# Kernel tuning notes

Measured on AMD Instinct MI355X. Metric: run time of the kernel, lower is better.

## Reference

```python
import jax, jax.numpy as jnp
import numpy as np

HEADS = 4
DIM_HEAD = 32
SCALE = 10.0  # scale=10 init arg
HIDDEN = HEADS * DIM_HEAD


def _l2norm(t, eps=1e-12):
    # matches torch F.normalize(t, dim=-1): normalize over last axis (flattened spatial)
    n = jnp.sqrt(jnp.sum(t * t, axis=-1, keepdims=True))
    return t / jnp.maximum(n, eps)


def setup_inputs() -> dict:
    key = jax.random.key(0)
    k1, k2, k3, k4, k5 = jax.random.split(key, 5)
    b, dim, H, W = 2, 128, 64, 64
    x = jax.random.normal(k1, (b, dim, H, W), jnp.float32)
    y = jax.random.normal(k2, (b, dim, H, W), jnp.float32)
    # to_qkv: Conv2d(dim, 3*hidden, 1, bias=False) -> weight (3*hidden, dim)
    w_qkv = jax.random.normal(k3, (3 * HIDDEN, dim), jnp.float32) / np.sqrt(dim)
    # to_out: Conv2d(hidden, dim, 1) -> weight (dim, hidden) + bias (dim,)
    w_out = jax.random.normal(k4, (dim, HIDDEN), jnp.float32) / np.sqrt(HIDDEN)
    b_out = jax.random.normal(k5, (dim,), jnp.float32) * 0.01
    return {"x": x, "y": y, "w_qkv": w_qkv, "w_out": w_out, "b_out": b_out}


def reference(x, y, w_qkv, w_out, b_out):
    b, c, H, W = x.shape
    n_x = H * W
    n_y = y.shape[2] * y.shape[3]
    xf = x.reshape(b, c, n_x)
    yf = y.reshape(b, c, n_y)
    # 1x1 conv == channel GEMM
    qkv_x = jnp.einsum('oc,bcn->bon', w_qkv, xf)
    qkv_y = jnp.einsum('oc,bcn->bon', w_qkv, yf)
    # only q from x, k/v from y are used downstream
    q_x = qkv_x[:, :HIDDEN].reshape(b, HEADS, DIM_HEAD, n_x)
    k_y = qkv_y[:, HIDDEN:2 * HIDDEN].reshape(b, HEADS, DIM_HEAD, n_y)
    v_y = qkv_y[:, 2 * HIDDEN:].reshape(b, HEADS, DIM_HEAD, n_y)
    q = _l2norm(q_x)
    k = _l2norm(k_y)
    sim = jnp.einsum('bhdi,bhdj->bhij', q, k) * SCALE  # [b,h,n_x,n_y]
    attn = jax.nn.softmax(sim, axis=-1)
    out = jnp.einsum('bhij,bhdj->bhdi', attn, v_y)  # [b,h,d,n_x]
    out = out.reshape(b, HIDDEN, H, W)  # 'b h (x y) d -> b (h d) x y'
    return jnp.einsum('oc,bcHW->boHW', w_out, out) + b_out[None, :, None, None]
```

## Files before the change

### kernel.cpp

```cpp
#include <hip/hip_runtime.h>
#include <hip/hip_bf16.h>

#define HEADS 4
#define DIMH  32
#define HID   128
#define DIM   128
#define NSP   4096
#define QSCALE_LOG2E 14.426950408889634f

typedef __attribute__((ext_vector_type(4)))  float f32x4;
typedef __attribute__((ext_vector_type(16))) float f32x16;
typedef __attribute__((ext_vector_type(8)))  short s16x8;

__device__ __forceinline__ unsigned cvtpk_bf16(float a, float b) {
  unsigned d;
  asm("v_cvt_pk_bf16_f32 %0, %1, %2" : "=v"(d) : "v"(a), "v"(b));
  return d;
}

__global__ __launch_bounds__(256) void k_cvt(const float* __restrict__ x,
                                             const float* __restrict__ y,
                                             __hip_bfloat16* __restrict__ xt,
                                             __hip_bfloat16* __restrict__ yt) {
  int bid = blockIdx.x;
  int t = bid >> 7, rem = bid & 127;
  int b = rem >> 6, nt = rem & 63;
  int n0 = nt * 64;
  const float* src = (t ? y : x) + (size_t)b * DIM * NSP;
  __hip_bfloat16* dst = (t ? yt : xt) + (size_t)b * NSP * DIM;

  __shared__ alignas(16) __hip_bfloat16 tile[64 * 136];
  int n = threadIdx.x & 63, c0 = threadIdx.x >> 6;
  const float* sp = src + n0 + n;
#pragma unroll
  for (int cc = 0; cc < 32; ++cc) {
    int c = cc * 4 + c0;
    tile[n * 136 + c] = __float2bfloat16(sp[(size_t)c * NSP]);
  }
  __syncthreads();
  int rrow = threadIdx.x >> 2, cb = (threadIdx.x & 3) * 32;
  __hip_bfloat16* op = dst + (size_t)(n0 + rrow) * DIM + cb;
  const __hip_bfloat16* ip = tile + rrow * 136 + cb;
#pragma unroll
  for (int k = 0; k < 4; ++k)
    *(s16x8*)(op + k * 8) = *(const s16x8*)(ip + k * 8);
}

__global__ __launch_bounds__(256, 4) void k_qkvm(const __hip_bfloat16* __restrict__ xt,
                                                 const __hip_bfloat16* __restrict__ yt,
                                                 const float* __restrict__ w,
                                                 float* __restrict__ ssp,
                                                 float* __restrict__ Qf,
                                                 __hip_bfloat16* __restrict__ Kr,
                                                 __hip_bfloat16* __restrict__ Vb) {
  int xcd = blockIdx.x & 7;
  int r = blockIdx.x >> 3;
  int ot = r >> 2;
  int nts = r & 3;
  int tile = xcd * 4 + nts;
  int n0 = tile * 256;
  int lane = threadIdx.x & 63, wave = threadIdx.x >> 6;
  int l31 = lane & 31, hi = lane >> 5;
  int orow = ot * 32 + l31;

  s16x8 wf[8];
  const float* wr = w + orow * DIM + hi * 8;
#pragma unroll
  for (int k = 0; k < 8; ++k) {
    f32x4 a = *(const f32x4*)(wr + k * 16);
    f32x4 b2 = *(const f32x4*)(wr + k * 16 + 4);
    union { unsigned u[4]; s16x8 v; } p;
    p.u[0] = cvtpk_bf16(a[0], a[1]);
    p.u[1] = cvtpk_bf16(a[2], a[3]);
    p.u[2] = cvtpk_bf16(b2[0], b2[1]);
    p.u[3] = cvtpk_bf16(b2[2], b2[3]);
    wf[k] = p.v;
  }

  const __hip_bfloat16* src = (ot < 4 ? xt : yt);
  int nw = n0 + wave * 64;
  f32x16 acc0 = {}, acc1 = {};
#pragma unroll
  for (int k = 0; k < 8; ++k) {
    s16x8 b0 = *(const s16x8*)(src + (size_t)(nw + l31) * DIM + k * 16 + hi * 8);
    s16x8 b1 = *(const s16x8*)(src + (size_t)(nw + 32 + l31) * DIM + k * 16 + hi * 8);
    acc0 = __builtin_amdgcn_mfma_f32_32x32x16_bf16(wf[k], b0, acc0, 0, 0, 0);
    acc1 = __builtin_amdgcn_mfma_f32_32x32x16_bf16(wf[k], b1, acc1, 0, 0, 0);
  }

  int b = nw >> 12;
  if (ot < 8) {
    int h = ot & 3;
    if (ot < 4) {
#pragma unroll
      for (int nt = 0; nt < 2; ++nt) {
        int np = (nw + nt * 32 + l31) & 4095;
        float* base = Qf + ((size_t)((b * HEADS + h) * NSP + np)) * DIMH;
        const f32x16& A = nt ? acc1 : acc0;
#pragma unroll
        for (int m = 0; m < 4; ++m) {
          f32x4 v = { A[4 * m], A[4 * m + 1], A[4 * m + 2], A[4 * m + 3] };
          *(f32x4*)(base + 8 * m + 4 * hi) = v;
        }
      }
    } else {
#pragma unroll
      for (int nt = 0; nt < 2; ++nt) {
        int np = (nw + nt * 32 + l31) & 4095;
        __hip_bfloat16* base = Kr + ((size_t)((b * HEADS + h) * NSP + np)) * DIMH;
        const f32x16& A = nt ? acc1 : acc0;
#pragma unroll
        for (int m = 0; m < 4; ++m) {
          uint2 p2;
          p2.x = cvtpk_bf16(A[4 * m], A[4 * m + 1]);
          p2.y = cvtpk_bf16(A[4 * m + 2], A[4 * m + 3]);
          *(uint2*)(base + 8 * m + 4 * hi) = p2;
        }
      }
    }
    float p[16];
#pragma unroll
    for (int r2 = 0; r2 < 16; ++r2) p[r2] = acc0[r2] * acc0[r2] + acc1[r2] * acc1[r2];
#pragma unroll
    for (int r2 = 0; r2 < 16; ++r2) {
#pragma unroll
      for (int m2 = 1; m2 < 32; m2 <<= 1) p[r2] += __shfl_xor(p[r2], m2);
    }
    if (l31 == 0) {
      int t = (ot < 4 ? 0 : 1);
      int widx = (tile & 15) * 4 + wave;
      int rbase = (t * 2 + b) * 128 + h * 32;
#pragma unroll
      for (int r2 = 0; r2 < 16; ++r2) {
        int row = (r2 & 3) + 8 * (r2 >> 2) + 4 * hi;
        ssp[(size_t)(rbase + row) * 64 + widx] = p[r2];
      }
    }
  } else {
    int h = ot - 8;
#pragma unroll
    for (int nt = 0; nt < 2; ++nt) {
      int np = (nw + nt * 32 + l31) & 4095;
      const f32x16& A = nt ? acc1 : acc0;
#pragma unroll
      for (int r2 = 0; r2 < 16; ++r2) {
        int d = (r2 & 3) + 8 * (r2 >> 2) + 4 * hi;
        Vb[((size_t)((b * HEADS + h) * DIMH + d)) * NSP + np] = __float2bfloat16(A[r2]);
      }
    }
  }
}

__device__ __forceinline__ void glds16(const __hip_bfloat16* g, __hip_bfloat16* l) {
  __builtin_amdgcn_global_load_lds(
      (const __attribute__((address_space(1))) unsigned int*)(const void*)g,
      (__attribute__((address_space(3))) unsigned int*)(void*)l, 16, 0, 0);
}

__device__ __forceinline__ void attn_sub2(const __hip_bfloat16* kbase,
                                          const __hip_bfloat16* vbase,
                                          int s, int l31, int hi,
                                          s16x8 qb0, s16x8 qb1,
                                          f32x16& O, float& lsum) {
  int krx = (l31 + (l31 >> 2)) & 3;
  int vrx = (l31 + (l31 >> 3)) & 7;
  const __hip_bfloat16* krow = kbase + (s * 32 + l31) * DIMH;
  s16x8 kf0 = *(const s16x8*)(krow + (((hi) ^ krx) << 3));
  s16x8 kf1 = *(const s16x8*)(krow + (((2 + hi) ^ krx) << 3));
  f32x16 z = {};
  f32x16 sv = __builtin_amdgcn_mfma_f32_32x32x16_bf16(kf0, qb0, z, 0, 0, 0);
  sv        = __builtin_amdgcn_mfma_f32_32x32x16_bf16(kf1, qb1, sv, 0, 0, 0);
  float p[16];
#pragma unroll
  for (int r = 0; r < 16; ++r) p[r] = __builtin_amdgcn_exp2f(sv[r]);
  float t0 = 0.f, t1 = 0.f;
#pragma unroll
  for (int r = 0; r < 16; r += 2) { t0 += p[r]; t1 += p[r + 1]; }
  lsum += t0 + t1;
  unsigned wA[4], wB[4];
#pragma unroll
  for (int m = 0; m < 4; ++m) {
    wA[m] = cvtpk_bf16(p[4 * m], p[4 * m + 1]);
    wB[m] = cvtpk_bf16(p[4 * m + 2], p[4 * m + 3]);
  }
  const __hip_bfloat16* vrow = vbase + l31 * 64;
#define PV_CHUNK(c2, vfrag)                                                    \
  {                                                                            \
    unsigned a0 = wA[2 * (c2)], a1 = wA[2 * (c2) + 1];                         \
    unsigned b0 = wB[2 * (c2)], b1 = wB[2 * (c2) + 1];                         \
    asm("v_permlane32_swap_b32 %0, %1" : "+v"(a0), "+v"(a1));                  \
    asm("v_permlane32_swap_b32 %0, %1" : "+v"(b0), "+v"(b1));                  \
    union { unsigned u[4]; s16x8 v; } pa;                                      \
    pa.u[0] = a0; pa.u[1] = b0; pa.u[2] = a1; pa.u[3] = b1;                    \
    O = __builtin_amdgcn_mfma_f32_32x32x16_bf16(pa.v, vfrag, O, 0, 0, 0);      \
  }
#pragma unroll
  for (int c2 = 0; c2 < 2; ++c2) {
    int cc = s * 2 + c2;
    s16x8 vf = *(const s16x8*)(vrow + (((cc * 2 + hi) ^ vrx) << 3));
    PV_CHUNK(c2, vf);
  }
#undef PV_CHUNK
}

__global__ __launch_bounds__(512, 4) void k_attn(const float* __restrict__ Qf,
                                                 const __hip_bfloat16* __restrict__ Kt,
                                                 const __hip_bfloat16* __restrict__ Vb,
                                                 const float* __restrict__ ssp,
                                                 __hip_bfloat16* __restrict__ Otb) {
  int bh = blockIdx.x & 7, qt = blockIdx.x >> 3;
  int tid = threadIdx.x, lane = tid & 63, wave = tid >> 6;
  int qsub = wave & 1, jq = wave >> 1;
  int l31 = lane & 31, hi = lane >> 5;
  int i0 = qt * 64 + qsub * 32;
  int jbase = jq * 1024;
  int b = bh >> 2, h = bh & 3;

  __shared__ alignas(16) char smem[65536];
  __shared__ float Llds[8][64];
  __shared__ float redl[64];
  __shared__ float fscl[32];
  __hip_bfloat16* KsB = (__hip_bfloat16*)smem;
  __hip_bfloat16* VsB = KsB + 16384;
  float* Olds = (float*)smem;

  {
    int row = tid >> 3, part = tid & 7;
    int qk = row >> 5, r32 = row & 31;
    const float* pp = ssp + (size_t)((qk * 2 + b) * 128 + h * 32 + r32) * 64 + part * 8;
    float s = 0.f;
#pragma unroll
    for (int k = 0; k < 8; ++k) s += pp[k];
    s += __shfl_xor(s, 1);
    s += __shfl_xor(s, 2);
    s += __shfl_xor(s, 4);
    if (part == 0) redl[row] = s;
  }
  __syncthreads();
  if (tid < 32) {
    float vq = 1.f / fmaxf(sqrtf(redl[tid]), 0.1f);
    float vk = 1.f / fmaxf(sqrtf(redl[tid + 32]), 0.1f);
    fscl[tid] = vq * vk * QSCALE_LOG2E;
  }
  __syncthreads();

  const __hip_bfloat16* kg = Kt + (size_t)bh * NSP * DIMH;
  const __hip_bfloat16* vg = Vb + (size_t)bh * DIMH * NSP;

  const float* qpf = Qf + ((size_t)bh * NSP + i0 + l31) * DIMH;
  s16x8 qb0, qb1;
  {
    f32x4 a0 = *(const f32x4*)(qpf + hi * 8);
    f32x4 a1 = *(const f32x4*)(qpf + hi * 8 + 4);
    f32x4 a2 = *(const f32x4*)(qpf + 16 + hi * 8);
    f32x4 a3 = *(const f32x4*)(qpf + 16 + hi * 8 + 4);
    f32x4 f0 = *(const f32x4*)(fscl + hi * 8);
    f32x4 f1 = *(const f32x4*)(fscl + hi * 8 + 4);
    f32x4 f2 = *(const f32x4*)(fscl + 16 + hi * 8);
    f32x4 f3 = *(const f32x4*)(fscl + 16 + hi * 8 + 4);
    union { unsigned u[4]; s16x8 v; } p0, p1;
    p0.u[0] = cvtpk_bf16(a0[0] * f0[0], a0[1] * f0[1]);
    p0.u[1] = cvtpk_bf16(a0[2] * f0[2], a0[3] * f0[3]);
    p0.u[2] = cvtpk_bf16(a1[0] * f1[0], a1[1] * f1[1]);
    p0.u[3] = cvtpk_bf16(a1[2] * f1[2], a1[3] * f1[3]);
    p1.u[0] = cvtpk_bf16(a2[0] * f2[0], a2[1] * f2[1]);
    p1.u[1] = cvtpk_bf16(a2[2] * f2[2], a2[3] * f2[3]);
    p1.u[2] = cvtpk_bf16(a3[0] * f3[0], a3[1] * f3[1]);
    p1.u[3] = cvtpk_bf16(a3[2] * f3[2], a3[3] * f3[3]);
    qb0 = p0.v; qb1 = p1.v;
  }

  int ku = qsub * 64 + lane;
  int krow = ku >> 2;
  int kch = (ku & 3) ^ ((krow + (krow >> 2)) & 3);
  const __hip_bfloat16* ksrc0 = kg + (size_t)krow * DIMH + (kch << 3);
  int vdA = ku >> 3;
  int vchA = (ku & 7) ^ ((vdA + (vdA >> 3)) & 7);
  const __hip_bfloat16* vsrcA = vg + (size_t)vdA * NSP + (vchA << 3);
  int vdB = vdA + 16;
  int vchB = (ku & 7) ^ ((vdB + (vdB >> 3)) & 7);
  const __hip_bfloat16* vsrcB = vg + (size_t)vdB * NSP + (vchB << 3);

  f32x16 O = {};
  float ls0 = 0.f, ls1 = 0.f;

#define STAGE(j0, buf)                                                         \
  {                                                                            \
    __hip_bfloat16* kd = KsB + (jq * 2 + (buf)) * 2048;                        \
    __hip_bfloat16* vd = VsB + (jq * 2 + (buf)) * 2048;                        \
    glds16(ksrc0 + (size_t)(j0) * DIMH,      kd + qsub * 512);                 \
    glds16(ksrc0 + (size_t)(j0 + 32) * DIMH, kd + 1024 + qsub * 512);          \
    glds16(vsrcA + (j0), vd + qsub * 512);                                     \
    glds16(vsrcB + (j0), vd + 1024 + qsub * 512);                              \
  }

  STAGE(jbase, 0);
  asm volatile("s_waitcnt vmcnt(0)" ::: "memory");
  __syncthreads();

#pragma unroll 1
  for (int t = 0; t < 16; ++t) {
    int buf = t & 1;
    if (t < 15) STAGE(jbase + (t + 1) * 64, buf ^ 1);
    const __hip_bfloat16* kbase = KsB + (jq * 2 + buf) * 2048;
    const __hip_bfloat16* vbase = VsB + (jq * 2 + buf) * 2048;
    attn_sub2(kbase, vbase, 0, l31, hi, qb0, qb1, O, ls0);
    attn_sub2(kbase, vbase, 1, l31, hi, qb0, qb1, O, ls1);
    if (t < 15) {
      asm volatile("s_waitcnt vmcnt(0)" ::: "memory");
      __syncthreads();
    }
  }
#undef STAGE

  float lsum = ls0 + ls1;
  float lw = lsum + __shfl_xor(lsum, 32);
  Llds[wave][lane] = lw;
  __syncthreads();
  if (jq) {
    float* od = Olds + (size_t)(qsub * 3 + (jq - 1)) * 1088;
#pragma unroll
    for (int r = 0; r < 16; ++r) od[r * 68 + lane] = O[r];
  }
  __syncthreads();
  if (jq == 0) {
    float ltot = lw + Llds[wave + 2][lane] + Llds[wave + 4][lane] + Llds[wave + 6][lane];
    if (hi == 0) Llds[wave][l31] = ltot;
    float* o0 = Olds + (size_t)(qsub * 3) * 1088;
    float* o1 = o0 + 1088;
    float* o2 = o1 + 1088;
#pragma unroll
    for (int r = 0; r < 16; ++r) {
      int i = (r & 3) + 8 * (r >> 2) + 4 * hi;
      float li = Llds[wave][i];
      float sum = O[r] + o0[r * 68 + lane] + o1[r * 68 + lane] + o2[r * 68 + lane];
      o0[r * 68 + lane] = sum / li;
    }
  }
  __syncthreads();
  {
    int q2 = tid >> 8;
    int i  = (tid >> 3) & 31;
    int cp = tid & 7;
    int r  = (i & 3) | ((i >> 3) << 2);
    int h2 = (i >> 2) & 1;
    const float* o0 = Olds + (size_t)(q2 * 3) * 1088 + r * 68 + h2 * 32 + cp * 4;
    uint2 pv;
    pv.x = cvtpk_bf16(o0[0], o0[1]);
    pv.y = cvtpk_bf16(o0[2], o0[3]);
    __hip_bfloat16* dst = Otb + ((size_t)(b * NSP + qt * 64 + q2 * 32 + i)) * HID + h * 32 + cp * 4;
    *(uint2*)dst = pv;
  }
}

__global__ __launch_bounds__(256, 4) void k_projm(const __hip_bfloat16* __restrict__ Otb,
                                                  const float* __restrict__ w,
                                                  const float* __restrict__ bias,
                                                  float* __restrict__ out) {
  int xcd = blockIdx.x & 7;
  int ot  = (blockIdx.x >> 3) & 3;
  int yy  = blockIdx.x >> 5;
  int tile = xcd * 8 + yy;
  int n0 = tile * 128;
  int lane = threadIdx.x & 63, wave = threadIdx.x >> 6;
  int l31 = lane & 31, hi = lane >> 5;
  int orow = ot * 32 + l31;

  s16x8 wf[8];
  const float* wr = w + orow * HID + hi * 8;
#pragma unroll
  for (int k = 0; k < 8; ++k) {
    f32x4 a = *(const f32x4*)(wr + k * 16);
    f32x4 b2 = *(const f32x4*)(wr + k * 16 + 4);
    union { unsigned u[4]; s16x8 v; } p;
    p.u[0] = cvtpk_bf16(a[0], a[1]);
    p.u[1] = cvtpk_bf16(a[2], a[3]);
    p.u[2] = cvtpk_bf16(b2[0], b2[1]);
    p.u[3] = cvtpk_bf16(b2[2], b2[3]);
    wf[k] = p.v;
  }

  int nw = n0 + wave * 32;
  int b = nw >> 12, np = nw & 4095;
  const __hip_bfloat16* src = Otb + ((size_t)(b * NSP + np)) * HID;
  f32x16 acc = {};
#pragma unroll
  for (int k = 0; k < 8; ++k) {
    s16x8 bfr = *(const s16x8*)(src + (size_t)l31 * HID + k * 16 + hi * 8);
    acc = __builtin_amdgcn_mfma_f32_32x32x16_bf16(wf[k], bfr, acc, 0, 0, 0);
  }

  float* outb = out + (size_t)b * DIM * NSP + np + l31;
#pragma unroll
  for (int r2 = 0; r2 < 16; ++r2) {
    int o = ot * 32 + (r2 & 3) + 8 * (r2 >> 2) + 4 * hi;
    outb[(size_t)o * NSP] = acc[r2] + bias[o];
  }
}

extern "C" void kernel_launch(void* const* d_in, const int* in_sizes, int n_in,
                              void* d_out, int out_size, void* d_ws, size_t ws_size,
                              hipStream_t stream) {
  const float* x     = (const float*)d_in[0];
  const float* y     = (const float*)d_in[1];
  const float* w_qkv = (const float*)d_in[2];
  const float* w_out = (const float*)d_in[3];
  const float* b_out = (const float*)d_in[4];
  float* out = (float*)d_out;

  char* ws = (char*)d_ws;
  __hip_bfloat16* xt  = (__hip_bfloat16*)(ws);
  __hip_bfloat16* yt  = (__hip_bfloat16*)(ws + (2  << 20));
  float* Qf           = (float*)(ws + (4  << 20));
  __hip_bfloat16* Kr  = (__hip_bfloat16*)(ws + (8  << 20));
  __hip_bfloat16* Vb  = (__hip_bfloat16*)(ws + (10 << 20));
  __hip_bfloat16* Otb = (__hip_bfloat16*)(ws + (12 << 20));
  float* ssp          = (float*)(ws + (16 << 20));

  k_cvt   <<<256, 256, 0, stream>>>(x, y, xt, yt);
  k_qkvm  <<<384, 256, 0, stream>>>(xt, yt, w_qkv, ssp, Qf, Kr, Vb);
  k_attn  <<<512, 512, 0, stream>>>(Qf, Kr, Vb, ssp, Otb);
  k_projm <<<256, 256, 0, stream>>>(Otb, w_out, b_out, out);
}
```

Measured before the change: 57.74 us.

## Widen attention blocks to 128 queries and triple-buffer K/V staging

The attention kernel now runs 1024-thread blocks covering 128 query rows (4 query sub-tiles × 4 key quarters). Each K/V tile is loaded cooperatively by four query waves, so every loaded tile is shared by more queries. Staging moves from double to triple buffering: loads are issued two tiles ahead, and each step waits with vmcnt(2) plus a raw s_barrier. The aim is to cut global K/V traffic per query and hide load latency better, at the cost of more LDS per block (about 96KB), fewer blocks (256) and possibly lower occupancy.

```diff
diff --git a/kernel.cpp b/kernel.cpp
--- a/kernel.cpp
+++ b/kernel.cpp
@@ -203,28 +203,28 @@
 #undef PV_CHUNK
 }
 
-__global__ __launch_bounds__(512, 4) void k_attn(const float* __restrict__ Qf,
-                                                 const __hip_bfloat16* __restrict__ Kt,
-                                                 const __hip_bfloat16* __restrict__ Vb,
-                                                 const float* __restrict__ ssp,
-                                                 __hip_bfloat16* __restrict__ Otb) {
+__global__ __launch_bounds__(1024, 4) void k_attn(const float* __restrict__ Qf,
+                                                  const __hip_bfloat16* __restrict__ Kt,
+                                                  const __hip_bfloat16* __restrict__ Vb,
+                                                  const float* __restrict__ ssp,
+                                                  __hip_bfloat16* __restrict__ Otb) {
   int bh = blockIdx.x & 7, qt = blockIdx.x >> 3;
   int tid = threadIdx.x, lane = tid & 63, wave = tid >> 6;
-  int qsub = wave & 1, jq = wave >> 1;
+  int qsub = wave & 3, jq = wave >> 2;
   int l31 = lane & 31, hi = lane >> 5;
-  int i0 = qt * 64 + qsub * 32;
+  int i0 = qt * 128 + qsub * 32;
   int jbase = jq * 1024;
   int b = bh >> 2, h = bh & 3;
 
-  __shared__ alignas(16) char smem[65536];
-  __shared__ float Llds[8][64];
+  __shared__ alignas(16) char smem[98304];
+  __shared__ float Llds[16][64];
   __shared__ float redl[64];
   __shared__ float fscl[32];
   __hip_bfloat16* KsB = (__hip_bfloat16*)smem;
-  __hip_bfloat16* VsB = KsB + 16384;
+  __hip_bfloat16* VsB = KsB + 24576;
   float* Olds = (float*)smem;
 
-  {
+  if (tid < 512) {
     int row = tid >> 3, part = tid & 7;
     int qk = row >> 5, r32 = row & 31;
     const float* pp = ssp + (size_t)((qk * 2 + b) * 128 + h * 32 + r32) * 64 + part * 8;
@@ -269,46 +269,45 @@
     p1.u[3] = cvtpk_bf16(a3[2] * f3[2], a3[3] * f3[3]);
     qb0 = p0.v; qb1 = p1.v;
   }
+  asm volatile("s_waitcnt vmcnt(0)" ::: "memory");
 
   int ku = qsub * 64 + lane;
   int krow = ku >> 2;
   int kch = (ku & 3) ^ ((krow + (krow >> 2)) & 3);
   const __hip_bfloat16* ksrc0 = kg + (size_t)krow * DIMH + (kch << 3);
-  int vdA = ku >> 3;
-  int vchA = (ku & 7) ^ ((vdA + (vdA >> 3)) & 7);
-  const __hip_bfloat16* vsrcA = vg + (size_t)vdA * NSP + (vchA << 3);
-  int vdB = vdA + 16;
-  int vchB = (ku & 7) ^ ((vdB + (vdB >> 3)) & 7);
-  const __hip_bfloat16* vsrcB = vg + (size_t)vdB * NSP + (vchB << 3);
+  int vd = ku >> 3;
+  int vch = (ku & 7) ^ ((vd + (vd >> 3)) & 7);
+  const __hip_bfloat16* vsrc0 = vg + (size_t)vd * NSP + (vch << 3);
+  int lbase = qsub * 512;
 
   f32x16 O = {};
   float ls0 = 0.f, ls1 = 0.f;
 
 #define STAGE(j0, buf)                                                         \
   {                                                                            \
-    __hip_bfloat16* kd = KsB + (jq * 2 + (buf)) * 2048;                        \
-    __hip_bfloat16* vd = VsB + (jq * 2 + (buf)) * 2048;                        \
-    glds16(ksrc0 + (size_t)(j0) * DIMH,      kd + qsub * 512);                 \
-    glds16(ksrc0 + (size_t)(j0 + 32) * DIMH, kd + 1024 + qsub * 512);          \
-    glds16(vsrcA + (j0), vd + qsub * 512);                                     \
-    glds16(vsrcB + (j0), vd + 1024 + qsub * 512);                              \
+    glds16(ksrc0 + (size_t)(j0) * DIMH, &KsB[(jq * 3 + (buf)) * 2048 + lbase]);\
+    glds16(vsrc0 + (j0),                &VsB[(jq * 3 + (buf)) * 2048 + lbase]);\
   }
 
   STAGE(jbase, 0);
-  asm volatile("s_waitcnt vmcnt(0)" ::: "memory");
+  STAGE(jbase + 64, 1);
+  asm volatile("s_waitcnt vmcnt(2)" ::: "memory");
   __syncthreads();
 
 #pragma unroll 1
   for (int t = 0; t < 16; ++t) {
-    int buf = t & 1;
-    if (t < 15) STAGE(jbase + (t + 1) * 64, buf ^ 1);
-    const __hip_bfloat16* kbase = KsB + (jq * 2 + buf) * 2048;
-    const __hip_bfloat16* vbase = VsB + (jq * 2 + buf) * 2048;
+    int bufc = t % 3;
+    if (t < 14) STAGE(jbase + (t + 2) * 64, (t + 2) % 3);
+    const __hip_bfloat16* kbase = &KsB[(jq * 3 + bufc) * 2048];
+    const __hip_bfloat16* vbase = &VsB[(jq * 3 + bufc) * 2048];
     attn_sub2(kbase, vbase, 0, l31, hi, qb0, qb1, O, ls0);
     attn_sub2(kbase, vbase, 1, l31, hi, qb0, qb1, O, ls1);
-    if (t < 15) {
+    if (t < 14) {
+      asm volatile("s_waitcnt vmcnt(2)" ::: "memory");
+      asm volatile("s_barrier" ::: "memory");
+    } else if (t < 15) {
       asm volatile("s_waitcnt vmcnt(0)" ::: "memory");
-      __syncthreads();
+      asm volatile("s_barrier" ::: "memory");
     }
   }
 #undef STAGE
@@ -324,7 +323,7 @@
   }
   __syncthreads();
   if (jq == 0) {
-    float ltot = lw + Llds[wave + 2][lane] + Llds[wave + 4][lane] + Llds[wave + 6][lane];
+    float ltot = lw + Llds[wave + 4][lane] + Llds[wave + 8][lane] + Llds[wave + 12][lane];
     if (hi == 0) Llds[wave][l31] = ltot;
     float* o0 = Olds + (size_t)(qsub * 3) * 1088;
     float* o1 = o0 + 1088;
@@ -348,7 +347,7 @@
     uint2 pv;
     pv.x = cvtpk_bf16(o0[0], o0[1]);
     pv.y = cvtpk_bf16(o0[2], o0[3]);
-    __hip_bfloat16* dst = Otb + ((size_t)(b * NSP + qt * 64 + q2 * 32 + i)) * HID + h * 32 + cp * 4;
+    __hip_bfloat16* dst = Otb + ((size_t)(b * NSP + qt * 128 + q2 * 32 + i)) * HID + h * 32 + cp * 4;
     *(uint2*)dst = pv;
   }
 }
@@ -417,8 +416,8 @@
   __hip_bfloat16* Otb = (__hip_bfloat16*)(ws + (12 << 20));
   float* ssp          = (float*)(ws + (16 << 20));
 
-  k_cvt   <<<256, 256, 0, stream>>>(x, y, xt, yt);
-  k_qkvm  <<<384, 256, 0, stream>>>(xt, yt, w_qkv, ssp, Qf, Kr, Vb);
-  k_attn  <<<512, 512, 0, stream>>>(Qf, Kr, Vb, ssp, Otb);
-  k_projm <<<256, 256, 0, stream>>>(Otb, w_out, b_out, out);
-}
+  k_cvt   <<<256, 256,  0, stream>>>(x, y, xt, yt);
+  k_qkvm  <<<384, 256,  0, stream>>>(xt, yt, w_qkv, ssp, Qf, Kr, Vb);
+  k_attn  <<<256, 1024, 0, stream>>>(Qf, Kr, Vb, ssp, Otb);
+  k_projm <<<256, 256,  0, stream>>>(Otb, w_out, b_out, out);
+}
```

Result: no change. 57.62 us (median of 2 runs) (-0.2%).
